# Kernel tuning notes

Hardware: AMD Instinct MI355X
Metric: run time of the kernel (lower is better)

The kernel has to match this reference:

```python
import jax, jax.numpy as jnp
import numpy as np
from jax import lax

COCO_80_TO_91 = [1,2,3,4,5,6,7,8,9,10,11,13,14,15,16,17,18,19,20,21,22,23,24,25,27,28,31,32,33,34,35,36,37,38,39,40,41,42,43,44,46,47,48,49,50,51,52,53,54,55,56,57,58,59,60,61,62,63,64,65,67,70,72,73,74,75,76,77,78,79,80,81,82,84,85,86,87,88,89,90]

CONF = 0.25      # self.confidence
IOU_THR = 0.7    # ultralytics NMS default
TOPK = 1000      # candidate cap before NMS
MAX_DET = 300    # ultralytics max_det default
MAX_WH = 7680.0  # per-class offset trick
IMG_SZ = 640.0   # yolov8 letterboxed input size


def setup_inputs() -> dict:
    key = jax.random.key(0)
    preds = jax.random.uniform(key, (32, 84, 8400), dtype=jnp.float32)
    return {"preds": preds}


def _nms_single(boxes, scores):
    """Greedy NMS on score-descending boxes [K,4] (class-offset xyxy). Returns keep mask [K]."""
    K = boxes.shape[0]
    area = (boxes[:, 2] - boxes[:, 0]) * (boxes[:, 3] - boxes[:, 1])  # [K]
    lt = jnp.maximum(boxes[:, None, :2], boxes[None, :, :2])          # [K,K,2]
    rb = jnp.minimum(boxes[:, None, 2:], boxes[None, :, 2:])
    wh = jnp.clip(rb - lt, 0.0)
    inter = wh[..., 0] * wh[..., 1]
    iou = inter / (area[:, None] + area[None, :] - inter + 1e-7)       # [K,K]
    idx = jnp.arange(K)
    sup = (iou > IOU_THR) & (idx[None, :] > idx[:, None])              # i suppresses later j

    def body(i, keep):
        return jnp.where(keep[i], keep & ~sup[i], keep)

    return lax.fori_loop(0, K, body, jnp.ones((K,), dtype=bool))


def reference(preds):
    # preds: [B, 84, N] -> [B, N, 84]
    p = jnp.transpose(preds, (0, 2, 1))
    box_xywh = p[..., :4] * IMG_SZ           # xywh in pixels on 640x640 canvas
    cls = p[..., 4:]                          # [B, N, 80]
    scores = jnp.max(cls, axis=-1)            # best-class confidence
    labels = jnp.argmax(cls, axis=-1)         # 0..79
    xy, wh = box_xywh[..., :2], box_xywh[..., 2:]
    xyxy = jnp.concatenate([xy - wh * 0.5, xy + wh * 0.5], axis=-1)  # decode

    # confidence filter + top-K candidate selection (score-descending)
    s_masked = jnp.where(scores > CONF, scores, -1.0)
    top_s, top_i = lax.top_k(s_masked, TOPK)                          # [B,TOPK]
    top_b = jnp.take_along_axis(xyxy, top_i[..., None], axis=1)      # [B,TOPK,4]
    top_l = jnp.take_along_axis(labels, top_i, axis=1)               # [B,TOPK]

    # per-class NMS via class offset
    off_b = top_b + (top_l.astype(top_b.dtype) * MAX_WH)[..., None]
    keep = jax.vmap(_nms_single)(off_b, top_s) & (top_s > CONF)

    # select final max_det detections, zero-pad invalid slots
    fin_s = jnp.where(keep, top_s, -1.0)
    out_s, out_i = lax.top_k(fin_s, MAX_DET)                          # [B,MAX_DET]
    out_b = jnp.take_along_axis(top_b, out_i[..., None], axis=1)
    out_l = jnp.take_along_axis(top_l, out_i, axis=1)
    valid = out_s > CONF
    boxes = jnp.where(valid[..., None], out_b, 0.0)
    scores_out = jnp.where(valid, out_s, 0.0)
    mapped = jnp.asarray(COCO_80_TO_91, dtype=jnp.int64)[out_l]       # COCO 80 -> 91 ids
    labels_out = jnp.where(valid, mapped, 0)
    return boxes, scores_out, labels_out
```

## Files before the change

kernel.cpp:

```cpp
#include <hip/hip_runtime.h>
#include <stdint.h>

typedef unsigned long long u64;
typedef unsigned int u32;

#define BATCH 32
#define NCH 84
#define NA 8400
#define NCLS 80
#define TOPK 1000
#define MAXDET 300
#define CONF 0.25f
#define IOU_T 0.7f
#define MAX_WH 7680.0f
#define IMG_SZ 640.0f
#define NT 1024
#define KPT 9
#define NCOPY 8
#define HPAD 260
#define DTILE 256

__device__ __constant__ float coco_map_f[NCLS] = {
    1,2,3,4,5,6,7,8,9,10,11,13,14,15,16,17,18,19,20,21,22,23,24,25,27,28,
    31,32,33,34,35,36,37,38,39,40,41,42,43,44,46,47,48,49,50,51,52,53,54,
    55,56,57,58,59,60,61,62,63,64,65,67,70,72,73,74,75,76,77,78,79,80,81,
    82,84,85,86,87,88,89,90};

__device__ inline u64 shflx64(u64 v, int m) {
    int lo = __shfl_xor((int)(u32)(v & 0xFFFFFFFFull), m, 64);
    int hi = __shfl_xor((int)(u32)(v >> 32), m, 64);
    return ((u64)(u32)hi << 32) | (u32)lo;
}

__global__ __launch_bounds__(256)
void decode_kernel(const float* __restrict__ preds,
                   u64* __restrict__ keys,
                   float4* __restrict__ boxes) {
    const int b = blockIdx.y;
    const int t = threadIdx.x;
    const int w = t >> 6, l = t & 63;
    const int wa = blockIdx.x * DTILE + w * 64;
    const int a = wa + l;
    const float* p = preds + (size_t)b * NCH * NA;

    __shared__ float stage[4][16][64];

    float bx = 0.f, by = 0.f, bw = 0.f, bh = 0.f;
    float best = -1.0f;
    int bl = 0;

    const int rsel = l >> 4;
    const int c4 = (l & 15) * 4;
    const int col = wa + c4;

    for (int chunk = 0; chunk < 6; ++chunk) {
        const int r0 = chunk * 16;
        const int nq = (chunk == 5) ? 1 : 4;
        for (int i = 0; i < nq; ++i) {
            int row = r0 + i * 4 + rsel;
            float4 v = (col < NA) ? *(const float4*)(p + (size_t)row * NA + col)
                                  : make_float4(0.f, 0.f, 0.f, 0.f);
            *(float4*)&stage[w][i * 4 + rsel][c4] = v;
        }
        __builtin_amdgcn_s_waitcnt(0xc07f);
        const int nr = (chunk == 5) ? 4 : 16;
        if (chunk == 0) {
            bx = stage[w][0][l]; by = stage[w][1][l];
            bw = stage[w][2][l]; bh = stage[w][3][l];
            best = stage[w][4][l]; bl = 0;
            for (int r = 5; r < 16; ++r) {
                float v = stage[w][r][l];
                int c = r - 4;
                bl = (v > best) ? c : bl;  best = fmaxf(v, best);
            }
        } else {
            for (int r = 0; r < nr; ++r) {
                float v = stage[w][r][l];
                int c = r0 + r - 4;
                bl = (v > best) ? c : bl;  best = fmaxf(v, best);
            }
        }
        __builtin_amdgcn_s_waitcnt(0xc07f);
    }

    if (a < NA) {
        float fx = bx * IMG_SZ, fy = by * IMG_SZ;
        float fw = bw * IMG_SZ, fh = bh * IMG_SZ;
        float hw = fw * 0.5f, hh = fh * 0.5f;
        boxes[(size_t)b * NA + a] = make_float4(fx - hw, fy - hh, fx + hw, fy + hh);
        float s = (best > CONF) ? best : -1.0f;
        u32 fb = __float_as_uint(s);
        u32 u = (fb & 0x80000000u) ? ~fb : (fb | 0x80000000u);
        keys[(size_t)b * NA + a] =
            ((u64)u << 21) | ((u64)(16383 - a) << 7) | (u64)bl;
    }
}

__global__ __launch_bounds__(NT)
void select_sort_kernel(const u64* __restrict__ keys,
                        const float4* __restrict__ boxes,
                        u64* __restrict__ sortedk,
                        float4* __restrict__ gbox,
                        unsigned short* __restrict__ grank,
                        int* __restrict__ gccnt) {
    const int b = blockIdx.x;
    const int t = threadIdx.x;
    const int lane = t & 63, wid = t >> 6;

    __shared__ union {
        struct {
            u64 sk[2][NT];
            int hist[NCOPY * HPAD];
        } a;
        struct {
            u64 cmask2[NCLS][16];
        } bb;
    } u_s;
    __shared__ int selB, selK, hselS, smax, scnt, cnt_s;

    u64 kreg[KPT];
    const u64* kb = keys + (size_t)b * NA;
    int nk = 0;
    for (int i = t; i < NA; i += NT) kreg[nk++] = kb[i];

    u64 P = 0ull;
    int kk = TOPK;
    int nsel = 0;
    for (int d = 3; d >= 0; --d) {
        const int sh = 21 + 8 * d;
        __syncthreads();
        if (t == 0) { smax = -1; scnt = 0; }
        __syncthreads();
        u64 hmask = (~0ull) << (sh + 8);
        int dig[KPT];
        int mymax = -1;
#pragma unroll
        for (int i = 0; i < KPT; ++i) {
            bool act = (i < nk) && (((kreg[i] ^ P) & hmask) == 0ull);
            dig[i] = act ? (int)((kreg[i] >> sh) & 255) : -1;
            mymax = max(mymax, dig[i]);
        }
#pragma unroll
        for (int off = 32; off; off >>= 1)
            mymax = max(mymax, __shfl_down(mymax, off, 64));
        if (lane == 0) atomicMax(&smax, mymax);
        __syncthreads();
        int maxb = smax;
        int myc = 0;
#pragma unroll
        for (int i = 0; i < KPT; ++i) myc += (dig[i] == maxb) ? 1 : 0;
#pragma unroll
        for (int off = 32; off; off >>= 1) myc += __shfl_down(myc, off, 64);
        if (lane == 0) atomicAdd(&scnt, myc);
        __syncthreads();
        int cm = scnt;
        if (cm >= kk) {
            P |= ((u64)maxb) << sh;
            nsel = TOPK - kk + cm;
            if (nsel <= NT) break;
            continue;
        }
        for (int i = t; i < NCOPY * HPAD; i += NT) u_s.a.hist[i] = 0;
        __syncthreads();
        int* myh = u_s.a.hist + (wid & (NCOPY - 1)) * HPAD;
#pragma unroll
        for (int i = 0; i < KPT; ++i)
            if (dig[i] >= 0) atomicAdd(&myh[dig[i]], 1);
        __syncthreads();
        if (t < 64) {
            int h0 = 0, h1 = 0, h2 = 0, h3 = 0;
            for (int c = 0; c < NCOPY; ++c) {
                const int* hp = u_s.a.hist + c * HPAD + 4 * t;
                h0 += hp[0]; h1 += hp[1]; h2 += hp[2]; h3 += hp[3];
            }
            int s = h0 + h1 + h2 + h3;
            int S = s;
            #pragma unroll
            for (int off = 1; off < 64; off <<= 1) {
                int o = __shfl_down(S, off, 64);
                if (t + off < 64) S += o;
            }
            int Snext = S - s;
            int c3 = Snext + h3, c2 = c3 + h2, c1 = c2 + h1, c0 = c1 + h0;
            int cand = -1, above = 0;
            if (c0 >= kk) {
                if      (c3 >= kk) { cand = 4 * t + 3; above = Snext; }
                else if (c2 >= kk) { cand = 4 * t + 2; above = c3; }
                else if (c1 >= kk) { cand = 4 * t + 1; above = c2; }
                else               { cand = 4 * t;     above = c1; }
            }
            int pc = (cand < 0) ? 0 : (((cand + 1) << 16) | (kk - above));
            #pragma unroll
            for (int off = 32; off; off >>= 1)
                pc = max(pc, __shfl_down(pc, off, 64));
            pc = __shfl(pc, 0, 64);
            int B = (pc >> 16) - 1;
            if (t == (B >> 2)) {
                int m4 = B & 3;
                selB = B;
                selK = pc & 0xFFFF;
                hselS = (m4 == 0) ? h0 : (m4 == 1) ? h1 : (m4 == 2) ? h2 : h3;
            }
        }
        __syncthreads();
        P |= ((u64)selB) << sh;
        kk = selK;
        nsel = TOPK - kk + hselS;
        if (nsel <= NT) break;
    }

    __syncthreads();
    if (t == 0) cnt_s = 0;
    __syncthreads();
    for (int i = 0; i < KPT; ++i) {
        bool p = (i < nk) && (kreg[i] >= P);
        u64 m = __ballot(p);
        int base = 0;
        if (lane == 0) base = atomicAdd(&cnt_s, (int)__popcll(m));
        base = __shfl(base, 0, 64);
        if (p) {
            int pos = base + (int)__popcll(m & ((1ull << lane) - 1ull));
            if (pos < NT) u_s.a.sk[0][pos] = kreg[i];
        }
    }
    if (t < NT - nsel) u_s.a.sk[0][nsel + t] = 0ull;
    __syncthreads();

    u64 myk = u_s.a.sk[0][t];
    int buf = 1;
    for (int size = 2; size <= NT; size <<= 1) {
        bool up = ((t & size) == 0);
        for (int stride = size >> 1; stride; stride >>= 1) {
            u64 pk;
            if (stride >= 64) {
                u_s.a.sk[buf][t] = myk;
                __syncthreads();
                pk = u_s.a.sk[buf][t ^ stride];
                buf ^= 1;
            } else {
                pk = shflx64(myk, stride);
            }
            bool tlow = ((t & stride) == 0);
            u64 mn = (myk < pk) ? myk : pk;
            u64 mx = (myk < pk) ? pk : myk;
            myk = up ? (tlow ? mx : mn) : (tlow ? mn : mx);
        }
    }
    sortedk[(size_t)b * NT + t] = myk;

    __syncthreads();
    for (int i = t; i < NCLS * 16; i += NT) ((u64*)u_s.bb.cmask2)[i] = 0ull;
    __syncthreads();

    int my_L = 0;
    float4 bx = make_float4(0.f, 0.f, 0.f, 0.f);
    if (t < TOPK) {
        int my_a = 16383 - (int)((myk >> 7) & 16383ull);
        my_L = (int)(myk & 127ull);
        bx = boxes[(size_t)b * NA + my_a];
        atomicOr(&u_s.bb.cmask2[my_L][t >> 6], 1ull << (t & 63));
    }
    __syncthreads();
    if (t < TOPK) {
        int w = t >> 6;
        int r = __popcll(u_s.bb.cmask2[my_L][w] & ((1ull << (t & 63)) - 1ull));
        for (int q = 0; q < w; ++q) r += __popcll(u_s.bb.cmask2[my_L][q]);
        gbox[(size_t)b * NT + t] = bx;
        if (r < 64) grank[((size_t)b * NCLS + my_L) * 64 + r] = (unsigned short)t;
    }
    if (t < NCLS) {
        int s = 0;
#pragma unroll
        for (int q = 0; q < 16; ++q) s += __popcll(u_s.bb.cmask2[t][q]);
        gccnt[(size_t)b * NCLS + t] = s;
    }
}

__global__ __launch_bounds__(NT)
void nms_epi_kernel(const u64* __restrict__ sortedk,
                    const float4* __restrict__ gbox,
                    const unsigned short* __restrict__ grank,
                    const int* __restrict__ gccnt,
                    float* __restrict__ out) {
    const int b = blockIdx.x;
    const int t = threadIdx.x;
    const int lane = t & 63, wid = t >> 6;

    __shared__ unsigned char keep[NT];
    __shared__ int wsum[16], woff[16], ktot_s;

    keep[t] = 0;

    int cnts[5];
#pragma unroll
    for (int j = 0; j < 5; ++j)
        cnts[j] = gccnt[(size_t)b * NCLS + wid + 16 * j];

    u64 myk = sortedk[(size_t)b * NT + t];
    __syncthreads();

    for (int j = 0; j < 5; ++j) {
        const int cc = wid + 16 * j;
        const int n = cnts[j];
        if (n == 0) continue;
        if (n <= 64) {
            float4 bbx = make_float4(0.f, 0.f, 0.f, 0.f);
            float aa = 0.f;
            int rk = 0;
            if (lane < n) {
                rk = grank[((size_t)b * NCLS + cc) * 64 + lane];
                float4 g = gbox[(size_t)b * NT + rk];
                float off = (float)cc * MAX_WH;
                bbx = make_float4(g.x + off, g.y + off, g.z + off, g.w + off);
                aa = (bbx.z - bbx.x) * (bbx.w - bbx.y);
            }
            u64 colm = 0ull;
            for (int i = 0; i < n; ++i) {
                float hx0 = __shfl(bbx.x, i, 64);
                float hy0 = __shfl(bbx.y, i, 64);
                float hx1 = __shfl(bbx.z, i, 64);
                float hy1 = __shfl(bbx.w, i, 64);
                float ha  = __shfl(aa, i, 64);
                float lx = fmaxf(hx0, bbx.x), ly = fmaxf(hy0, bbx.y);
                float rx = fminf(hx1, bbx.z), ry = fminf(hy1, bbx.w);
                float w = fmaxf(rx - lx, 0.0f);
                float h = fmaxf(ry - ly, 0.0f);
                float inter = w * h;
                float denom = ha + aa;
                denom = denom - inter;
                denom = denom + 1e-7f;
                bool s = (lane > i) && (lane < n) && (inter / denom > IOU_T);
                colm |= ((u64)s) << i;
            }
            u64 alive = (n >= 64) ? ~0ull : ((1ull << n) - 1ull);
            for (int i = 0; i < n; ++i) {
                if (!((alive >> i) & 1ull)) continue;
                alive &= ~__ballot((colm >> i) & 1ull);
            }
            if (lane < n) keep[rk] = (unsigned char)((alive >> lane) & 1ull);
        } else if (lane == 0) {
            const u64* skb = sortedk + (size_t)b * NT;
            const float4* gb = gbox + (size_t)b * NT;
            const float off = (float)cc * MAX_WH;
            u64 aliveW[16];
            for (int q = 0; q < 16; ++q) aliveW[q] = ~0ull;
            for (int i = 0; i < TOPK; ++i) {
                if ((int)(skb[i] & 127ull) != cc) continue;
                if (!((aliveW[i >> 6] >> (i & 63)) & 1ull)) continue;
                float4 g = gb[i];
                float ix0 = g.x + off, iy0 = g.y + off;
                float ix1 = g.z + off, iy1 = g.w + off;
                float ai = (ix1 - ix0) * (iy1 - iy0);
                for (int jj = i + 1; jj < TOPK; ++jj) {
                    if ((int)(skb[jj] & 127ull) != cc) continue;
                    if (!((aliveW[jj >> 6] >> (jj & 63)) & 1ull)) continue;
                    float4 h = gb[jj];
                    float jx0 = h.x + off, jy0 = h.y + off;
                    float jx1 = h.z + off, jy1 = h.w + off;
                    float aj = (jx1 - jx0) * (jy1 - jy0);
                    float lx = fmaxf(ix0, jx0), ly = fmaxf(iy0, jy0);
                    float rx = fminf(ix1, jx1), ry = fminf(iy1, jy1);
                    float ww = fmaxf(rx - lx, 0.0f);
                    float hh = fmaxf(ry - ly, 0.0f);
                    float inter = ww * hh;
                    float denom = ai + aj;
                    denom = denom - inter;
                    denom = denom + 1e-7f;
                    if (inter / denom > IOU_T) aliveW[jj >> 6] &= ~(1ull << (jj & 63));
                }
            }
            for (int i = 0; i < TOPK; ++i)
                if ((int)(skb[i] & 127ull) == cc)
                    keep[i] = (unsigned char)((aliveW[i >> 6] >> (i & 63)) & 1ull);
        }
    }
    __syncthreads();

    float sj = 0.0f;
    bool valid = false;
    if (t < TOPK) {
        u32 u = (u32)(myk >> 21);
        u32 fb = (u & 0x80000000u) ? (u ^ 0x80000000u) : ~u;
        sj = __uint_as_float(fb);
        valid = keep[t] && (sj > CONF);
    }
    u64 m = __ballot(valid);
    if (lane == 0) wsum[wid] = (int)__popcll(m);
    __syncthreads();
    if (wid == 0) {
        int v = (lane < 16) ? wsum[lane] : 0;
        #pragma unroll
        for (int o = 1; o < 16; o <<= 1) {
            int x = __shfl_up(v, o, 64);
            if (lane >= o) v += x;
        }
        if (lane < 16) woff[lane] = v - wsum[lane];
        if (lane == 15) ktot_s = v;
    }
    __syncthreads();
    int ktot = ktot_s;
    int rank = woff[wid] + (int)__popcll(m & ((1ull << lane) - 1ull));

    float* out_boxes = out;
    float* out_scores = out + (size_t)BATCH * MAXDET * 4;
    float* out_labels = out + (size_t)BATCH * MAXDET * 5;
    if (valid && rank < MAXDET) {
        float4 bx = gbox[(size_t)b * NT + t];
        float* ob = out_boxes + ((size_t)b * MAXDET + rank) * 4;
        ob[0] = bx.x; ob[1] = bx.y; ob[2] = bx.z; ob[3] = bx.w;
        out_scores[(size_t)b * MAXDET + rank] = sj;
        out_labels[(size_t)b * MAXDET + rank] = coco_map_f[(int)(myk & 127ull)];
    }
    if (t < MAXDET && t >= ktot) {
        float* ob = out_boxes + ((size_t)b * MAXDET + t) * 4;
        ob[0] = 0.0f; ob[1] = 0.0f; ob[2] = 0.0f; ob[3] = 0.0f;
        out_scores[(size_t)b * MAXDET + t] = 0.0f;
        out_labels[(size_t)b * MAXDET + t] = 0.0f;
    }
}

extern "C" void kernel_launch(void* const* d_in, const int* in_sizes, int n_in,
                              void* d_out, int out_size, void* d_ws, size_t ws_size,
                              hipStream_t stream) {
    const float* preds = (const float*)d_in[0];
    char* ws = (char*)d_ws;
    size_t off = 0;
    auto alloc = [&](size_t bytes) { char* p = ws + off; off += (bytes + 255) & ~(size_t)255; return p; };

    u64* keys            = (u64*)           alloc((size_t)BATCH * NA * 8);
    float4* boxes        = (float4*)        alloc((size_t)BATCH * NA * 16);
    u64* sortedk         = (u64*)           alloc((size_t)BATCH * NT * 8);
    float4* gbox         = (float4*)        alloc((size_t)BATCH * NT * 16);
    unsigned short* grank= (unsigned short*)alloc((size_t)BATCH * NCLS * 64 * 2);
    int* gccnt           = (int*)           alloc((size_t)BATCH * NCLS * 4);
    float* out = (float*)d_out;

    dim3 dgrid((NA + DTILE - 1) / DTILE, BATCH);
    decode_kernel<<<dgrid, 256, 0, stream>>>(preds, keys, boxes);
    select_sort_kernel<<<BATCH, NT, 0, stream>>>(keys, boxes, sortedk,
                                                 gbox, grank, gccnt);
    nms_epi_kernel<<<BATCH, NT, 0, stream>>>(sortedk, gbox, grank, gccnt, out);
}
```

Before: 184.1 us.

## Split per-class NMS into its own grid and simplify decode loads

Per-class NMS moves out of the fused NMS+epilogue kernel into its own kernel with one 64-thread block per (class, batch). Each keep flag goes to global memory, and a separate epilogue kernel compacts the survivors. The select kernel now precomputes the class-offset boxes and areas for each class slot. The decode kernel drops its LDS staging and reads the strided channels directly per anchor, and the select kernel gets an occupancy hint. The aim is to spread the serial per-class NMS loops over many more compute units, at the cost of an extra kernel launch and a global round trip for the keep flags.

```diff
diff --git a/kernel.cpp b/kernel.cpp
--- a/kernel.cpp
+++ b/kernel.cpp
@@ -18,7 +18,6 @@
 #define KPT 9
 #define NCOPY 8
 #define HPAD 260
-#define DTILE 256
 
 __device__ __constant__ float coco_map_f[NCLS] = {
     1,2,3,4,5,6,7,8,9,10,11,13,14,15,16,17,18,19,20,21,22,23,24,25,27,28,
@@ -37,53 +36,27 @@
                    u64* __restrict__ keys,
                    float4* __restrict__ boxes) {
     const int b = blockIdx.y;
-    const int t = threadIdx.x;
-    const int w = t >> 6, l = t & 63;
-    const int wa = blockIdx.x * DTILE + w * 64;
-    const int a = wa + l;
-    const float* p = preds + (size_t)b * NCH * NA;
-
-    __shared__ float stage[4][16][64];
-
-    float bx = 0.f, by = 0.f, bw = 0.f, bh = 0.f;
+    const int a = blockIdx.x * 256 + threadIdx.x;
+    const bool live = (a < NA);
+    const int ac = live ? a : (NA - 1);
+    const float* p = preds + (size_t)b * NCH * NA + ac;
+
+    float bx = p[0];
+    float by = p[(size_t)1 * NA];
+    float bw = p[(size_t)2 * NA];
+    float bh = p[(size_t)3 * NA];
+
+    const float* pc = p + (size_t)4 * NA;
     float best = -1.0f;
     int bl = 0;
-
-    const int rsel = l >> 4;
-    const int c4 = (l & 15) * 4;
-    const int col = wa + c4;
-
-    for (int chunk = 0; chunk < 6; ++chunk) {
-        const int r0 = chunk * 16;
-        const int nq = (chunk == 5) ? 1 : 4;
-        for (int i = 0; i < nq; ++i) {
-            int row = r0 + i * 4 + rsel;
-            float4 v = (col < NA) ? *(const float4*)(p + (size_t)row * NA + col)
-                                  : make_float4(0.f, 0.f, 0.f, 0.f);
-            *(float4*)&stage[w][i * 4 + rsel][c4] = v;
-        }
-        __builtin_amdgcn_s_waitcnt(0xc07f);
-        const int nr = (chunk == 5) ? 4 : 16;
-        if (chunk == 0) {
-            bx = stage[w][0][l]; by = stage[w][1][l];
-            bw = stage[w][2][l]; bh = stage[w][3][l];
-            best = stage[w][4][l]; bl = 0;
-            for (int r = 5; r < 16; ++r) {
-                float v = stage[w][r][l];
-                int c = r - 4;
-                bl = (v > best) ? c : bl;  best = fmaxf(v, best);
-            }
-        } else {
-            for (int r = 0; r < nr; ++r) {
-                float v = stage[w][r][l];
-                int c = r0 + r - 4;
-                bl = (v > best) ? c : bl;  best = fmaxf(v, best);
-            }
-        }
-        __builtin_amdgcn_s_waitcnt(0xc07f);
-    }
-
-    if (a < NA) {
+#pragma unroll 16
+    for (int r = 0; r < NCLS; ++r) {
+        float v = pc[(size_t)r * NA];
+        bl = (v > best) ? r : bl;
+        best = fmaxf(v, best);
+    }
+
+    if (live) {
         float fx = bx * IMG_SZ, fy = by * IMG_SZ;
         float fw = bw * IMG_SZ, fh = bh * IMG_SZ;
         float hw = fw * 0.5f, hh = fh * 0.5f;
@@ -96,11 +69,13 @@
     }
 }
 
-__global__ __launch_bounds__(NT)
+__global__ __launch_bounds__(NT, 4)
 void select_sort_kernel(const u64* __restrict__ keys,
                         const float4* __restrict__ boxes,
                         u64* __restrict__ sortedk,
                         float4* __restrict__ gbox,
+                        float4* __restrict__ goffb,
+                        float* __restrict__ garea,
                         unsigned short* __restrict__ grank,
                         int* __restrict__ gccnt) {
     const int b = blockIdx.x;
@@ -120,8 +95,11 @@
 
     u64 kreg[KPT];
     const u64* kb = keys + (size_t)b * NA;
-    int nk = 0;
-    for (int i = t; i < NA; i += NT) kreg[nk++] = kb[i];
+#pragma unroll
+    for (int j = 0; j < KPT; ++j) {
+        int i = t + j * NT;
+        kreg[j] = (i < NA) ? kb[i] : 0ull;
+    }
 
     u64 P = 0ull;
     int kk = TOPK;
@@ -135,10 +113,10 @@
         int dig[KPT];
         int mymax = -1;
 #pragma unroll
-        for (int i = 0; i < KPT; ++i) {
-            bool act = (i < nk) && (((kreg[i] ^ P) & hmask) == 0ull);
-            dig[i] = act ? (int)((kreg[i] >> sh) & 255) : -1;
-            mymax = max(mymax, dig[i]);
+        for (int j = 0; j < KPT; ++j) {
+            bool act = (((kreg[j] ^ P) & hmask) == 0ull) && (kreg[j] != 0ull);
+            dig[j] = act ? (int)((kreg[j] >> sh) & 255) : -1;
+            mymax = max(mymax, dig[j]);
         }
 #pragma unroll
         for (int off = 32; off; off >>= 1)
@@ -148,7 +126,7 @@
         int maxb = smax;
         int myc = 0;
 #pragma unroll
-        for (int i = 0; i < KPT; ++i) myc += (dig[i] == maxb) ? 1 : 0;
+        for (int j = 0; j < KPT; ++j) myc += (dig[j] == maxb) ? 1 : 0;
 #pragma unroll
         for (int off = 32; off; off >>= 1) myc += __shfl_down(myc, off, 64);
         if (lane == 0) atomicAdd(&scnt, myc);
@@ -164,8 +142,8 @@
         __syncthreads();
         int* myh = u_s.a.hist + (wid & (NCOPY - 1)) * HPAD;
 #pragma unroll
-        for (int i = 0; i < KPT; ++i)
-            if (dig[i] >= 0) atomicAdd(&myh[dig[i]], 1);
+        for (int j = 0; j < KPT; ++j)
+            if (dig[j] >= 0) atomicAdd(&myh[dig[j]], 1);
         __syncthreads();
         if (t < 64) {
             int h0 = 0, h1 = 0, h2 = 0, h3 = 0;
@@ -212,15 +190,16 @@
     __syncthreads();
     if (t == 0) cnt_s = 0;
     __syncthreads();
-    for (int i = 0; i < KPT; ++i) {
-        bool p = (i < nk) && (kreg[i] >= P);
+#pragma unroll
+    for (int j = 0; j < KPT; ++j) {
+        bool p = (kreg[j] >= P);
         u64 m = __ballot(p);
         int base = 0;
         if (lane == 0) base = atomicAdd(&cnt_s, (int)__popcll(m));
         base = __shfl(base, 0, 64);
         if (p) {
             int pos = base + (int)__popcll(m & ((1ull << lane) - 1ull));
-            if (pos < NT) u_s.a.sk[0][pos] = kreg[i];
+            if (pos < NT) u_s.a.sk[0][pos] = kreg[j];
         }
     }
     if (t < NT - nsel) u_s.a.sk[0][nsel + t] = 0ull;
@@ -266,7 +245,15 @@
         int r = __popcll(u_s.bb.cmask2[my_L][w] & ((1ull << (t & 63)) - 1ull));
         for (int q = 0; q < w; ++q) r += __popcll(u_s.bb.cmask2[my_L][q]);
         gbox[(size_t)b * NT + t] = bx;
-        if (r < 64) grank[((size_t)b * NCLS + my_L) * 64 + r] = (unsigned short)t;
+        if (r < 64) {
+            float off = (float)my_L * MAX_WH;
+            float ox0 = bx.x + off, oy0 = bx.y + off;
+            float ox1 = bx.z + off, oy1 = bx.w + off;
+            size_t ci = ((size_t)b * NCLS + my_L) * 64 + r;
+            goffb[ci] = make_float4(ox0, oy0, ox1, oy1);
+            garea[ci] = (ox1 - ox0) * (oy1 - oy0);
+            grank[ci] = (unsigned short)t;
+        }
     }
     if (t < NCLS) {
         int s = 0;
@@ -276,113 +263,105 @@
     }
 }
 
+__global__ __launch_bounds__(64)
+void nms_kernel(const float4* __restrict__ goffb,
+                const float* __restrict__ garea,
+                const unsigned short* __restrict__ grank,
+                const int* __restrict__ gccnt,
+                const u64* __restrict__ sortedk,
+                const float4* __restrict__ gbox,
+                unsigned char* __restrict__ keepg) {
+    const int c = blockIdx.x;
+    const int b = blockIdx.y;
+    const int lane = threadIdx.x;
+    const int n = gccnt[(size_t)b * NCLS + c];
+    if (n == 0) return;
+
+    if (n <= 64) {
+        size_t ci = ((size_t)b * NCLS + c) * 64 + lane;
+        float4 bb = make_float4(0.f, 0.f, 0.f, 0.f);
+        float ar = 0.f;
+        int rk = 0;
+        if (lane < n) { bb = goffb[ci]; ar = garea[ci]; rk = grank[ci]; }
+        u64 colm = 0ull;
+        for (int i = 0; i < n; ++i) {
+            float hx0 = __shfl(bb.x, i, 64);
+            float hy0 = __shfl(bb.y, i, 64);
+            float hx1 = __shfl(bb.z, i, 64);
+            float hy1 = __shfl(bb.w, i, 64);
+            float ha  = __shfl(ar, i, 64);
+            float lx = fmaxf(hx0, bb.x), ly = fmaxf(hy0, bb.y);
+            float rx = fminf(hx1, bb.z), ry = fminf(hy1, bb.w);
+            float w = fmaxf(rx - lx, 0.0f);
+            float h = fmaxf(ry - ly, 0.0f);
+            float inter = w * h;
+            float denom = ha + ar;
+            denom = denom - inter;
+            denom = denom + 1e-7f;
+            bool s = (lane > i) && (lane < n) && (inter / denom > IOU_T);
+            colm |= ((u64)s) << i;
+        }
+        u64 alive = (n >= 64) ? ~0ull : ((1ull << n) - 1ull);
+        for (int i = 0; i < n; ++i) {
+            if (!((alive >> i) & 1ull)) continue;
+            alive &= ~__ballot((colm >> i) & 1ull);
+        }
+        if (lane < n) keepg[(size_t)b * NT + rk] = (unsigned char)((alive >> lane) & 1ull);
+    } else if (lane == 0) {
+        const u64* skb = sortedk + (size_t)b * NT;
+        const float4* gb = gbox + (size_t)b * NT;
+        const float off = (float)c * MAX_WH;
+        u64 aliveW[16];
+        for (int q = 0; q < 16; ++q) aliveW[q] = ~0ull;
+        for (int i = 0; i < TOPK; ++i) {
+            if ((int)(skb[i] & 127ull) != c) continue;
+            if (!((aliveW[i >> 6] >> (i & 63)) & 1ull)) continue;
+            float4 g = gb[i];
+            float ix0 = g.x + off, iy0 = g.y + off;
+            float ix1 = g.z + off, iy1 = g.w + off;
+            float ai = (ix1 - ix0) * (iy1 - iy0);
+            for (int jj = i + 1; jj < TOPK; ++jj) {
+                if ((int)(skb[jj] & 127ull) != c) continue;
+                if (!((aliveW[jj >> 6] >> (jj & 63)) & 1ull)) continue;
+                float4 h = gb[jj];
+                float jx0 = h.x + off, jy0 = h.y + off;
+                float jx1 = h.z + off, jy1 = h.w + off;
+                float aj = (jx1 - jx0) * (jy1 - jy0);
+                float lx = fmaxf(ix0, jx0), ly = fmaxf(iy0, jy0);
+                float rx = fminf(ix1, jx1), ry = fminf(iy1, jy1);
+                float ww = fmaxf(rx - lx, 0.0f);
+                float hh = fmaxf(ry - ly, 0.0f);
+                float inter = ww * hh;
+                float denom = ai + aj;
+                denom = denom - inter;
+                denom = denom + 1e-7f;
+                if (inter / denom > IOU_T) aliveW[jj >> 6] &= ~(1ull << (jj & 63));
+            }
+        }
+        for (int i = 0; i < TOPK; ++i)
+            if ((int)(skb[i] & 127ull) == c)
+                keepg[(size_t)b * NT + i] = (unsigned char)((aliveW[i >> 6] >> (i & 63)) & 1ull);
+    }
+}
+
 __global__ __launch_bounds__(NT)
-void nms_epi_kernel(const u64* __restrict__ sortedk,
-                    const float4* __restrict__ gbox,
-                    const unsigned short* __restrict__ grank,
-                    const int* __restrict__ gccnt,
-                    float* __restrict__ out) {
+void epilogue_kernel(const u64* __restrict__ sortedk,
+                     const unsigned char* __restrict__ keepg,
+                     const float4* __restrict__ gbox,
+                     float* __restrict__ out) {
     const int b = blockIdx.x;
     const int t = threadIdx.x;
     const int lane = t & 63, wid = t >> 6;
-
-    __shared__ unsigned char keep[NT];
     __shared__ int wsum[16], woff[16], ktot_s;
 
-    keep[t] = 0;
-
-    int cnts[5];
-#pragma unroll
-    for (int j = 0; j < 5; ++j)
-        cnts[j] = gccnt[(size_t)b * NCLS + wid + 16 * j];
-
     u64 myk = sortedk[(size_t)b * NT + t];
-    __syncthreads();
-
-    for (int j = 0; j < 5; ++j) {
-        const int cc = wid + 16 * j;
-        const int n = cnts[j];
-        if (n == 0) continue;
-        if (n <= 64) {
-            float4 bbx = make_float4(0.f, 0.f, 0.f, 0.f);
-            float aa = 0.f;
-            int rk = 0;
-            if (lane < n) {
-                rk = grank[((size_t)b * NCLS + cc) * 64 + lane];
-                float4 g = gbox[(size_t)b * NT + rk];
-                float off = (float)cc * MAX_WH;
-                bbx = make_float4(g.x + off, g.y + off, g.z + off, g.w + off);
-                aa = (bbx.z - bbx.x) * (bbx.w - bbx.y);
-            }
-            u64 colm = 0ull;
-            for (int i = 0; i < n; ++i) {
-                float hx0 = __shfl(bbx.x, i, 64);
-                float hy0 = __shfl(bbx.y, i, 64);
-                float hx1 = __shfl(bbx.z, i, 64);
-                float hy1 = __shfl(bbx.w, i, 64);
-                float ha  = __shfl(aa, i, 64);
-                float lx = fmaxf(hx0, bbx.x), ly = fmaxf(hy0, bbx.y);
-                float rx = fminf(hx1, bbx.z), ry = fminf(hy1, bbx.w);
-                float w = fmaxf(rx - lx, 0.0f);
-                float h = fmaxf(ry - ly, 0.0f);
-                float inter = w * h;
-                float denom = ha + aa;
-                denom = denom - inter;
-                denom = denom + 1e-7f;
-                bool s = (lane > i) && (lane < n) && (inter / denom > IOU_T);
-                colm |= ((u64)s) << i;
-            }
-            u64 alive = (n >= 64) ? ~0ull : ((1ull << n) - 1ull);
-            for (int i = 0; i < n; ++i) {
-                if (!((alive >> i) & 1ull)) continue;
-                alive &= ~__ballot((colm >> i) & 1ull);
-            }
-            if (lane < n) keep[rk] = (unsigned char)((alive >> lane) & 1ull);
-        } else if (lane == 0) {
-            const u64* skb = sortedk + (size_t)b * NT;
-            const float4* gb = gbox + (size_t)b * NT;
-            const float off = (float)cc * MAX_WH;
-            u64 aliveW[16];
-            for (int q = 0; q < 16; ++q) aliveW[q] = ~0ull;
-            for (int i = 0; i < TOPK; ++i) {
-                if ((int)(skb[i] & 127ull) != cc) continue;
-                if (!((aliveW[i >> 6] >> (i & 63)) & 1ull)) continue;
-                float4 g = gb[i];
-                float ix0 = g.x + off, iy0 = g.y + off;
-                float ix1 = g.z + off, iy1 = g.w + off;
-                float ai = (ix1 - ix0) * (iy1 - iy0);
-                for (int jj = i + 1; jj < TOPK; ++jj) {
-                    if ((int)(skb[jj] & 127ull) != cc) continue;
-                    if (!((aliveW[jj >> 6] >> (jj & 63)) & 1ull)) continue;
-                    float4 h = gb[jj];
-                    float jx0 = h.x + off, jy0 = h.y + off;
-                    float jx1 = h.z + off, jy1 = h.w + off;
-                    float aj = (jx1 - jx0) * (jy1 - jy0);
-                    float lx = fmaxf(ix0, jx0), ly = fmaxf(iy0, jy0);
-                    float rx = fminf(ix1, jx1), ry = fminf(iy1, jy1);
-                    float ww = fmaxf(rx - lx, 0.0f);
-                    float hh = fmaxf(ry - ly, 0.0f);
-                    float inter = ww * hh;
-                    float denom = ai + aj;
-                    denom = denom - inter;
-                    denom = denom + 1e-7f;
-                    if (inter / denom > IOU_T) aliveW[jj >> 6] &= ~(1ull << (jj & 63));
-                }
-            }
-            for (int i = 0; i < TOPK; ++i)
-                if ((int)(skb[i] & 127ull) == cc)
-                    keep[i] = (unsigned char)((aliveW[i >> 6] >> (i & 63)) & 1ull);
-        }
-    }
-    __syncthreads();
-
+    bool valid = false;
     float sj = 0.0f;
-    bool valid = false;
     if (t < TOPK) {
         u32 u = (u32)(myk >> 21);
         u32 fb = (u & 0x80000000u) ? (u ^ 0x80000000u) : ~u;
         sj = __uint_as_float(fb);
-        valid = keep[t] && (sj > CONF);
+        valid = keepg[(size_t)b * NT + t] && (sj > CONF);
     }
     u64 m = __ballot(valid);
     if (lane == 0) wsum[wid] = (int)__popcll(m);
@@ -390,9 +369,9 @@
     if (wid == 0) {
         int v = (lane < 16) ? wsum[lane] : 0;
         #pragma unroll
-        for (int o = 1; o < 16; o <<= 1) {
-            int x = __shfl_up(v, o, 64);
-            if (lane >= o) v += x;
+        for (int off = 1; off < 16; off <<= 1) {
+            int o = __shfl_up(v, off, 64);
+            if (lane >= off) v += o;
         }
         if (lane < 16) woff[lane] = v - wsum[lane];
         if (lane == 15) ktot_s = v;
@@ -431,13 +410,19 @@
     float4* boxes        = (float4*)        alloc((size_t)BATCH * NA * 16);
     u64* sortedk         = (u64*)           alloc((size_t)BATCH * NT * 8);
     float4* gbox         = (float4*)        alloc((size_t)BATCH * NT * 16);
+    float4* goffb        = (float4*)        alloc((size_t)BATCH * NCLS * 64 * 16);
+    float* garea         = (float*)         alloc((size_t)BATCH * NCLS * 64 * 4);
     unsigned short* grank= (unsigned short*)alloc((size_t)BATCH * NCLS * 64 * 2);
     int* gccnt           = (int*)           alloc((size_t)BATCH * NCLS * 4);
+    unsigned char* keepg = (unsigned char*) alloc((size_t)BATCH * NT);
     float* out = (float*)d_out;
 
-    dim3 dgrid((NA + DTILE - 1) / DTILE, BATCH);
+    dim3 dgrid((NA + 255) / 256, BATCH);
     decode_kernel<<<dgrid, 256, 0, stream>>>(preds, keys, boxes);
-    select_sort_kernel<<<BATCH, NT, 0, stream>>>(keys, boxes, sortedk,
-                                                 gbox, grank, gccnt);
-    nms_epi_kernel<<<BATCH, NT, 0, stream>>>(sortedk, gbox, grank, gccnt, out);
-}
+    select_sort_kernel<<<BATCH, NT, 0, stream>>>(keys, boxes, sortedk, gbox,
+                                                 goffb, garea, grank, gccnt);
+    dim3 ngrid(NCLS, BATCH);
+    nms_kernel<<<ngrid, 64, 0, stream>>>(goffb, garea, grank, gccnt,
+                                         sortedk, gbox, keepg);
+    epilogue_kernel<<<BATCH, NT, 0, stream>>>(sortedk, keepg, gbox, out);
+}
```

New measurement: 164.2 us. 10.8% less time.
